# Kernel tuning notes

Hardware: AMD Instinct MI355X
Metric: run time of the kernel (lower is better)

## Reference

```python
import jax, jax.numpy as jnp
import numpy as np
import math

B, T, C, H = 2, 2048, 1024, 16
DH = C // H  # head_dim = 64
NEG = -1000000000.0


def _rope_freqs(T, half, base=10000.0):
    inv = 1.0 / (base ** (np.arange(0, half, dtype=np.float32) * 2.0 / (2 * half)))
    ang = np.arange(T, dtype=np.float32)[:, None] * inv[None, :]  # (T, half)
    return np.cos(ang)[None, :, None, :], np.sin(ang)[None, :, None, :]


def setup_inputs() -> dict:
    key = jax.random.key(0)
    ks = jax.random.split(key, 9)
    s = 1.0 / math.sqrt(C)
    cos, sin = _rope_freqs(T, DH // 2)
    return {
        "x": jax.random.normal(ks[0], (B, T, C), jnp.float32),
        "mask": jnp.tril(jnp.ones((T, T), bool))[None, None],  # (1,1,T,T) causal
        "freqs_cos": jnp.asarray(cos),
        "freqs_sin": jnp.asarray(sin),
        "wq": jax.random.normal(ks[1], (C, C), jnp.float32) * s,
        "bq": jnp.zeros((C,), jnp.float32),
        "wk": jax.random.normal(ks[2], (C, C), jnp.float32) * s,
        "bk": jnp.zeros((C,), jnp.float32),
        "wv": jax.random.normal(ks[3], (C, C), jnp.float32) * s,
        "bv": jnp.zeros((C,), jnp.float32),
        "wo": jax.random.normal(ks[4], (C, C), jnp.float32) * s,
        "bo": jnp.zeros((C,), jnp.float32),
    }


def _apply_rope(x, cos, sin):
    # x: (B, T, H, D); cos/sin: (1, T, 1, D/2)
    xr, xi = x[..., 0::2], x[..., 1::2]
    rr = xr * cos - xi * sin
    ri = xr * sin + xi * cos
    b, t, h, _ = x.shape
    return jnp.stack([rr, ri], axis=-1).reshape(b, t, h, x.shape[-1])


def reference(x, mask, freqs_cos, freqs_sin, wq, bq, wk, bk, wv, bv, wo, bo):
    b, t, c = x.shape
    q = (x @ wq + bq).reshape(b, t, H, DH)
    k = (x @ wk + bk).reshape(b, t, H, DH)
    v = (x @ wv + bv).reshape(b, t, H, DH)
    q = _apply_rope(q, freqs_cos, freqs_sin)
    k = _apply_rope(k, freqs_cos, freqs_sin)
    scores = jnp.einsum('bqhd,bkhd->bhqk', q, k) / math.sqrt(DH)
    scores = jnp.where(mask, scores, NEG)
    probs = jax.nn.softmax(scores, axis=-1)  # dropout is identity (deterministic)
    out = jnp.einsum('bhqk,bkhd->bqhd', probs, v).reshape(b, t, c)
    return out @ wo + bo
```

## Files before the change

### kernel.cpp

```cpp
#include <hip/hip_runtime.h>
#include <hip/hip_bf16.h>


typedef __attribute__((ext_vector_type(8))) short bf16x8;
typedef __attribute__((ext_vector_type(4))) float f32x4;
typedef unsigned short u16;

#define DEV __device__ __forceinline__

#define GLDS16(g, l)                                                        \
  __builtin_amdgcn_global_load_lds(                                         \
      (const __attribute__((address_space(1))) void*)(g),                   \
      (__attribute__((address_space(3))) void*)(l), 16, 0, 0)

DEV u16 f2bf(float f) {
  __hip_bfloat16 h = __float2bfloat16(f);
  u16 u; __builtin_memcpy(&u, &h, 2); return u;
}

__global__ __launch_bounds__(256) void k_cvt(const float* __restrict__ in,
                                             u16* __restrict__ out) {
  int i = (blockIdx.x * 256 + threadIdx.x) * 8;
  float4 a = *(const float4*)(in + i);
  float4 b = *(const float4*)(in + i + 4);
  union { u16 us[8]; uint4 v; } pk;
  pk.us[0] = f2bf(a.x); pk.us[1] = f2bf(a.y); pk.us[2] = f2bf(a.z); pk.us[3] = f2bf(a.w);
  pk.us[4] = f2bf(b.x); pk.us[5] = f2bf(b.y); pk.us[6] = f2bf(b.z); pk.us[7] = f2bf(b.w);
  *(uint4*)(out + i) = pk.v;
}

__global__ __launch_bounds__(256) void k_trw(const float* __restrict__ wq,
                                             const float* __restrict__ wk,
                                             const float* __restrict__ wv,
                                             const float* __restrict__ wo,
                                             u16* __restrict__ Wt,
                                             u16* __restrict__ Wot) {
  __shared__ float tile[32][33];
  const int z = blockIdx.z;
  const float* src = (z == 0) ? wq : (z == 1) ? wk : (z == 2) ? wv : wo;
  u16* dst = (z < 3) ? (Wt + (size_t)z * 1024 * 1024) : Wot;
  const int n0 = blockIdx.x * 32, k0 = blockIdx.y * 32;
  const int tx = threadIdx.x & 31, ty = threadIdx.x >> 5;
#pragma unroll
  for (int rr = 0; rr < 4; ++rr) {
    int k = ty + rr * 8;
    tile[k][tx] = src[(size_t)(k0 + k) * 1024 + n0 + tx];
  }
  __syncthreads();
#pragma unroll
  for (int rr = 0; rr < 4; ++rr) {
    int n = ty + rr * 8;
    dst[(size_t)(n0 + n) * 1024 + k0 + tx] = f2bf(tile[tx][n]);
  }
}

__global__ __launch_bounds__(256) void k_trv(const u16* __restrict__ Vg,
                                             u16* __restrict__ Vt) {
  __shared__ u16 tile[64][72];
  const int tid = threadIdx.x;
  const int bh = blockIdx.y;
  const int t0 = blockIdx.x * 64;
  const int r = tid >> 2, q = tid & 3;
  const u16* src = &Vg[((size_t)bh * 2048 + t0 + r) * 64 + q * 16];
  uint4 u0 = *(const uint4*)src;
  uint4 u1 = *(const uint4*)(src + 8);
  *(uint4*)&tile[r][q * 16] = u0;
  *(uint4*)&tile[r][q * 16 + 8] = u1;
  __syncthreads();
  const int d = tid >> 2;
  union { u16 us[16]; uint4 v[2]; } pk;
#pragma unroll
  for (int i = 0; i < 16; ++i) pk.us[i] = tile[q * 16 + i][d];
  u16* dst = &Vt[((size_t)bh * 64 + d) * 2048 + t0 + q * 16];
  *(uint4*)dst = pk.v[0];
  *(uint4*)(dst + 8) = pk.v[1];
}

template <int EPI>
__global__ __launch_bounds__(256) void k_gemm(
    const u16* __restrict__ A, const u16* __restrict__ Bt,
    const float* __restrict__ b0, const float* __restrict__ b1,
    const float* __restrict__ b2, const float* __restrict__ fcos,
    const float* __restrict__ fsin, u16* __restrict__ Qg, u16* __restrict__ Kg,
    u16* __restrict__ Vg, float* __restrict__ outF) {
  __shared__ u16 As[128 * 32];
  __shared__ u16 Bs[128 * 32];
  const int tid = threadIdx.x, lane = tid & 63, wid = tid >> 6;
  const int wm = wid >> 1, wn = wid & 1;
  const int lr = lane & 15, lg = lane >> 4;
  const int m0 = blockIdx.y * 128, n0 = blockIdx.x * 128;
  const int K = 1024;
  f32x4 acc[4][4] = {};

  const int srcChunk = (lane & 3) ^ ((lane >> 3) & 3);
  const int rowIn = lane >> 2;
  const int seg0 = wid * 2;
  const u16* aSrc0 = &A[(size_t)(m0 + seg0 * 16 + rowIn) * K + srcChunk * 8];
  const u16* aSrc1 = aSrc0 + 16 * K;
  const u16* bSrc0 = &Bt[(size_t)(n0 + seg0 * 16 + rowIn) * K + srcChunk * 8];
  const u16* bSrc1 = bSrc0 + 16 * K;
  u16* aDst0 = &As[seg0 * 512];
  u16* aDst1 = &As[seg0 * 512 + 512];
  u16* bDst0 = &Bs[seg0 * 512];
  u16* bDst1 = &Bs[seg0 * 512 + 512];

  const int slot = (lg ^ ((lr >> 1) & 3)) * 8;

  for (int kt = 0; kt < 32; ++kt) {
    const int ko = kt * 32;
    GLDS16(aSrc0 + ko, aDst0);
    GLDS16(aSrc1 + ko, aDst1);
    GLDS16(bSrc0 + ko, bDst0);
    GLDS16(bSrc1 + ko, bDst1);
    __syncthreads();
    bf16x8 af[4], bfr[4];
#pragma unroll
    for (int i = 0; i < 4; ++i)
      af[i] = *(const bf16x8*)&As[(wm * 64 + i * 16 + lr) * 32 + slot];
#pragma unroll
    for (int j = 0; j < 4; ++j)
      bfr[j] = *(const bf16x8*)&Bs[(wn * 64 + j * 16 + lr) * 32 + slot];
#pragma unroll
    for (int i = 0; i < 4; ++i)
#pragma unroll
      for (int j = 0; j < 4; ++j)
        acc[i][j] = __builtin_amdgcn_mfma_f32_16x16x32_bf16(af[i], bfr[j],
                                                            acc[i][j], 0, 0, 0);
    __syncthreads();
  }

  if constexpr (EPI == 0) {
#pragma unroll
    for (int i = 0; i < 4; ++i) {
#pragma unroll
      for (int j = 0; j < 4; ++j) {
        f32x4 v = acc[i][j];
        int n = n0 + wn * 64 + j * 16 + lr;
        int mat = n >> 10, nn = n & 1023;
        int h = nn >> 6, d = nn & 63;
        float bval = (mat == 0 ? b0 : (mat == 1 ? b1 : b2))[nn];
        int mb = m0 + wm * 64 + i * 16 + lg * 4;
        if (mat < 2) {
          int p = d >> 1;
          float sgn = (d & 1) ? 1.0f : -1.0f;
          u16* dst = (mat == 0) ? Qg : Kg;
#pragma unroll
          for (int r = 0; r < 4; ++r) {
            int m = mb + r, t = m & 2047, b = m >> 11;
            float val = v[r] + bval;
            float c = fcos[t * 32 + p], s = fsin[t * 32 + p];
            float partner = __shfl_xor(val, 1);
            float rv = val * c + sgn * partner * s;
            dst[((size_t)(b * 16 + h) * 2048 + t) * 64 + d] = f2bf(rv);
          }
        } else {
#pragma unroll
          for (int r = 0; r < 4; ++r) {
            int m = mb + r, t = m & 2047, b = m >> 11;
            Vg[((size_t)(b * 16 + h) * 2048 + t) * 64 + d] = f2bf(v[r] + bval);
          }
        }
      }
    }
  } else {
#pragma unroll
    for (int i = 0; i < 4; ++i) {
#pragma unroll
      for (int j = 0; j < 4; ++j) {
        int n = n0 + wn * 64 + j * 16 + lr;
        float bval = b0[n];
        int mb = m0 + wm * 64 + i * 16 + lg * 4;
#pragma unroll
        for (int r = 0; r < 4; ++r)
          outF[(size_t)(mb + r) * 1024 + n] = acc[i][j][r] + bval;
      }
    }
  }
}

__global__ __launch_bounds__(256, 2) void k_attn(const u16* __restrict__ Qg,
                                                 const u16* __restrict__ Kg,
                                                 const u16* __restrict__ Vt,
                                                 u16* __restrict__ Ab) {
  __shared__ u16 PA_lds[4][16][72];
  __shared__ u16 PB_lds[4][16][72];
  const int tid = threadIdx.x, lane = tid & 63, w = tid >> 6;
  const int lr = lane & 15, lg = lane >> 4;
  const int iA = blockIdx.x;
  const int iB = 31 - iA;
  const int bh = blockIdx.y;
  const size_t qkbase = (size_t)bh * 2048 * 64;
  const int qrowA = iA * 64 + w * 16;
  const int qrowB = iB * 64 + w * 16;

  bf16x8 aQA[2], aQB[2];
#pragma unroll
  for (int c = 0; c < 2; ++c) {
    aQA[c] = *(const bf16x8*)&Qg[qkbase + (size_t)(qrowA + lr) * 64 + lg * 8 + c * 32];
    aQB[c] = *(const bf16x8*)&Qg[qkbase + (size_t)(qrowB + lr) * 64 + lg * 8 + c * 32];
  }

  f32x4 accA[4] = {}, accB[4] = {};
  float mA[4], lA[4], mB[4], lB[4];
#pragma unroll
  for (int r = 0; r < 4; ++r) { mA[r] = -1e30f; lA[r] = 0.f; mB[r] = -1e30f; lB[r] = 0.f; }

  bf16x8 k0buf[4][2], k1buf[4][2];
#pragma unroll
  for (int nt = 0; nt < 4; ++nt) {
    const u16* kp = &Kg[qkbase + (size_t)(nt * 16 + lr) * 64 + lg * 8];
    k0buf[nt][0] = *(const bf16x8*)kp;
    k0buf[nt][1] = *(const bf16x8*)(kp + 32);
  }

  auto chain = [&](float (&p)[4][4], float (&m_run)[4], float (&l_run)[4],
                   f32x4 (&acc_o)[4], u16 (&P_lds)[4][16][72]) {
    float pm[4], alpha[4], rs[4];
#pragma unroll
    for (int r = 0; r < 4; ++r)
      pm[r] = fmaxf(fmaxf(p[0][r], p[1][r]), fmaxf(p[2][r], p[3][r]));
#pragma unroll
    for (int off = 1; off < 16; off <<= 1)
#pragma unroll
      for (int r = 0; r < 4; ++r) pm[r] = fmaxf(pm[r], __shfl_xor(pm[r], off));
#pragma unroll
    for (int r = 0; r < 4; ++r) {
      float mn = fmaxf(m_run[r], pm[r]);
      alpha[r] = __expf(m_run[r] - mn);
      m_run[r] = mn;
    }
#pragma unroll
    for (int nt = 0; nt < 4; ++nt)
#pragma unroll
      for (int r = 0; r < 4; ++r) p[nt][r] = __expf(p[nt][r] - m_run[r]);
#pragma unroll
    for (int r = 0; r < 4; ++r) rs[r] = (p[0][r] + p[1][r]) + (p[2][r] + p[3][r]);
#pragma unroll
    for (int off = 1; off < 16; off <<= 1)
#pragma unroll
      for (int r = 0; r < 4; ++r) rs[r] += __shfl_xor(rs[r], off);
#pragma unroll
    for (int r = 0; r < 4; ++r) l_run[r] = l_run[r] * alpha[r] + rs[r];
#pragma unroll
    for (int j = 0; j < 4; ++j)
#pragma unroll
      for (int r = 0; r < 4; ++r) acc_o[j][r] *= alpha[r];
#pragma unroll
    for (int nt = 0; nt < 4; ++nt)
#pragma unroll
      for (int r = 0; r < 4; ++r)
        P_lds[w][lg * 4 + r][nt * 16 + lr] = f2bf(p[nt][r]);
  };

  auto step = [&](bf16x8 (&kcur)[4][2], bf16x8 (&knxt)[4][2], int kt) {
    const int kv0 = kt * 64;
    const bool doA = (kt <= iA);
    f32x4 sB[4], sA[4];
#pragma unroll
    for (int nt = 0; nt < 4; ++nt) {
      f32x4 s = {};
      s = __builtin_amdgcn_mfma_f32_16x16x32_bf16(aQB[0], kcur[nt][0], s, 0, 0, 0);
      s = __builtin_amdgcn_mfma_f32_16x16x32_bf16(aQB[1], kcur[nt][1], s, 0, 0, 0);
      sB[nt] = s;
    }
    if (doA) {
#pragma unroll
      for (int nt = 0; nt < 4; ++nt) {
        f32x4 s = {};
        s = __builtin_amdgcn_mfma_f32_16x16x32_bf16(aQA[0], kcur[nt][0], s, 0, 0, 0);
        s = __builtin_amdgcn_mfma_f32_16x16x32_bf16(aQA[1], kcur[nt][1], s, 0, 0, 0);
        sA[nt] = s;
      }
    }
    if (kt < iB) {
#pragma unroll
      for (int nt = 0; nt < 4; ++nt) {
        const u16* kp = &Kg[qkbase + (size_t)(kv0 + 64 + nt * 16 + lr) * 64 + lg * 8];
        knxt[nt][0] = *(const bf16x8*)kp;
        knxt[nt][1] = *(const bf16x8*)(kp + 32);
      }
    }
    bf16x8 vc[4][2];
#pragma unroll
    for (int j = 0; j < 4; ++j) {
      const u16* vp = &Vt[(size_t)(bh * 64 + j * 16 + lr) * 2048 + kv0 + lg * 8];
      vc[j][0] = *(const bf16x8*)vp;
      vc[j][1] = *(const bf16x8*)(vp + 32);
    }
    float pB[4][4], pA[4][4];
#pragma unroll
    for (int nt = 0; nt < 4; ++nt)
#pragma unroll
      for (int r = 0; r < 4; ++r) {
        float xB = sB[nt][r] * 0.125f;
        if (kt == iB && (kv0 + nt * 16 + lr > qrowB + lg * 4 + r)) xB = -1e30f;
        pB[nt][r] = xB;
      }
    if (doA) {
#pragma unroll
      for (int nt = 0; nt < 4; ++nt)
#pragma unroll
        for (int r = 0; r < 4; ++r) {
          float xA = sA[nt][r] * 0.125f;
          if (kt == iA && (kv0 + nt * 16 + lr > qrowA + lg * 4 + r)) xA = -1e30f;
          pA[nt][r] = xA;
        }
    }
    chain(pB, mB, lB, accB, PB_lds);
    if (doA) chain(pA, mA, lA, accA, PA_lds);
    asm volatile("s_waitcnt lgkmcnt(0)" ::: "memory");
    __builtin_amdgcn_sched_barrier(0);
    bf16x8 aPB0 = *(const bf16x8*)&PB_lds[w][lr][lg * 8];
    bf16x8 aPB1 = *(const bf16x8*)&PB_lds[w][lr][lg * 8 + 32];
#pragma unroll
    for (int j = 0; j < 4; ++j) {
      accB[j] = __builtin_amdgcn_mfma_f32_16x16x32_bf16(aPB0, vc[j][0], accB[j], 0, 0, 0);
      accB[j] = __builtin_amdgcn_mfma_f32_16x16x32_bf16(aPB1, vc[j][1], accB[j], 0, 0, 0);
    }
    if (doA) {
      bf16x8 aPA0 = *(const bf16x8*)&PA_lds[w][lr][lg * 8];
      bf16x8 aPA1 = *(const bf16x8*)&PA_lds[w][lr][lg * 8 + 32];
#pragma unroll
      for (int j = 0; j < 4; ++j) {
        accA[j] = __builtin_amdgcn_mfma_f32_16x16x32_bf16(aPA0, vc[j][0], accA[j], 0, 0, 0);
        accA[j] = __builtin_amdgcn_mfma_f32_16x16x32_bf16(aPA1, vc[j][1], accA[j], 0, 0, 0);
      }
    }
  };

  int kt = 0;
  while (true) {
    step(k0buf, k1buf, kt);
    ++kt; if (kt > iB) break;
    step(k1buf, k0buf, kt);
    ++kt; if (kt > iB) break;
  }

  const int b = bh >> 4, h = bh & 15;
#pragma unroll
  for (int j = 0; j < 4; ++j)
#pragma unroll
    for (int r = 0; r < 4; ++r) {
      int qA = qrowA + lg * 4 + r;
      int qB = qrowB + lg * 4 + r;
      Ab[(size_t)(b * 2048 + qA) * 1024 + h * 64 + j * 16 + lr] = f2bf(accA[j][r] / lA[r]);
      Ab[(size_t)(b * 2048 + qB) * 1024 + h * 64 + j * 16 + lr] = f2bf(accB[j][r] / lB[r]);
    }
}

extern "C" void kernel_launch(void* const* d_in, const int* in_sizes, int n_in,
                              void* d_out, int out_size, void* d_ws,
                              size_t ws_size, hipStream_t stream) {
  (void)in_sizes; (void)n_in; (void)out_size; (void)ws_size;
  const float* x = (const float*)d_in[0];
  const float* fcos = (const float*)d_in[2];
  const float* fsin = (const float*)d_in[3];
  const float* wq = (const float*)d_in[4];
  const float* bq = (const float*)d_in[5];
  const float* wk = (const float*)d_in[6];
  const float* bk = (const float*)d_in[7];
  const float* wv = (const float*)d_in[8];
  const float* bv = (const float*)d_in[9];
  const float* wo = (const float*)d_in[10];
  const float* bo = (const float*)d_in[11];
  float* out = (float*)d_out;
  char* ws = (char*)d_ws;
  const size_t MB = 1024 * 1024;
  u16* Xb  = (u16*)(ws);
  u16* Wt  = (u16*)(ws + 8 * MB);
  u16* Wot = (u16*)(ws + 14 * MB);
  u16* Qg  = (u16*)(ws + 16 * MB);
  u16* Kg  = (u16*)(ws + 24 * MB);
  u16* Vg  = (u16*)(ws + 32 * MB);
  u16* Vt  = (u16*)(ws + 40 * MB);
  u16* Ab  = Xb;

  k_cvt<<<2048, 256, 0, stream>>>(x, Xb);
  k_trw<<<dim3(32, 32, 4), 256, 0, stream>>>(wq, wk, wv, wo, Wt, Wot);
  k_gemm<0><<<dim3(24, 32), 256, 0, stream>>>(Xb, Wt, bq, bk, bv, fcos, fsin,
                                              Qg, Kg, Vg, nullptr);
  k_trv<<<dim3(32, 32), 256, 0, stream>>>(Vg, Vt);
  k_attn<<<dim3(16, 32), 256, 0, stream>>>(Qg, Kg, Vt, Ab);
  k_gemm<1><<<dim3(8, 32), 256, 0, stream>>>(Ab, Wot, bo, nullptr, nullptr,
                                             nullptr, nullptr, nullptr, nullptr,
                                             nullptr, out);
}
```

Measured before the change: 288.2 us.

## Split KV tiles across two warp halves in attention and merge partial softmax

The attention block grows from 256 to 512 threads. The two halves of the warps take even and odd KV tiles, and each prefetches K two tiles ahead. After the loop, the odd half writes its partial accumulators and running max/sum to LDS, reusing the P buffers. The even half then rescales and merges them before writing the output. This doubles the waves working on each query pair, which should raise latency hiding and shorten per-block serial work; the costs are an extra LDS combine step and two barriers. The tighter launch bound of (512,4) may also cap registers hard enough to cause spills.

```diff
diff --git a/kernel.cpp b/kernel.cpp
--- a/kernel.cpp
+++ b/kernel.cpp
@@ -178,20 +178,26 @@
   }
 }
 
-__global__ __launch_bounds__(256, 2) void k_attn(const u16* __restrict__ Qg,
+struct CombW {
+  float acc[2][16][65];
+  float ml[2][2][16];
+};
+__global__ __launch_bounds__(512, 4) void k_attn(const u16* __restrict__ Qg,
                                                  const u16* __restrict__ Kg,
                                                  const u16* __restrict__ Vt,
                                                  u16* __restrict__ Ab) {
-  __shared__ u16 PA_lds[4][16][72];
-  __shared__ u16 PB_lds[4][16][72];
+  __shared__ u16 P_all[2][8][16][72];
   const int tid = threadIdx.x, lane = tid & 63, w = tid >> 6;
+  const int wl = w & 3, half = w >> 2;
   const int lr = lane & 15, lg = lane >> 4;
   const int iA = blockIdx.x;
   const int iB = 31 - iA;
   const int bh = blockIdx.y;
   const size_t qkbase = (size_t)bh * 2048 * 64;
-  const int qrowA = iA * 64 + w * 16;
-  const int qrowB = iB * 64 + w * 16;
+  const int qrowA = iA * 64 + wl * 16;
+  const int qrowB = iB * 64 + wl * 16;
+  u16 (*PA)[72] = P_all[0][w];
+  u16 (*PB)[72] = P_all[1][w];
 
   bf16x8 aQA[2], aQB[2];
 #pragma unroll
@@ -208,13 +214,13 @@
   bf16x8 k0buf[4][2], k1buf[4][2];
 #pragma unroll
   for (int nt = 0; nt < 4; ++nt) {
-    const u16* kp = &Kg[qkbase + (size_t)(nt * 16 + lr) * 64 + lg * 8];
+    const u16* kp = &Kg[qkbase + (size_t)(half * 64 + nt * 16 + lr) * 64 + lg * 8];
     k0buf[nt][0] = *(const bf16x8*)kp;
     k0buf[nt][1] = *(const bf16x8*)(kp + 32);
   }
 
   auto chain = [&](float (&p)[4][4], float (&m_run)[4], float (&l_run)[4],
-                   f32x4 (&acc_o)[4], u16 (&P_lds)[4][16][72]) {
+                   f32x4 (&acc_o)[4], u16 (*P)[72]) {
     float pm[4], alpha[4], rs[4];
 #pragma unroll
     for (int r = 0; r < 4; ++r)
@@ -249,7 +255,7 @@
     for (int nt = 0; nt < 4; ++nt)
 #pragma unroll
       for (int r = 0; r < 4; ++r)
-        P_lds[w][lg * 4 + r][nt * 16 + lr] = f2bf(p[nt][r]);
+        P[lg * 4 + r][nt * 16 + lr] = f2bf(p[nt][r]);
   };
 
   auto step = [&](bf16x8 (&kcur)[4][2], bf16x8 (&knxt)[4][2], int kt) {
@@ -272,10 +278,10 @@
         sA[nt] = s;
       }
     }
-    if (kt < iB) {
+    if (kt + 2 <= iB) {
 #pragma unroll
       for (int nt = 0; nt < 4; ++nt) {
-        const u16* kp = &Kg[qkbase + (size_t)(kv0 + 64 + nt * 16 + lr) * 64 + lg * 8];
+        const u16* kp = &Kg[qkbase + (size_t)(kv0 + 128 + nt * 16 + lr) * 64 + lg * 8];
         knxt[nt][0] = *(const bf16x8*)kp;
         knxt[nt][1] = *(const bf16x8*)(kp + 32);
       }
@@ -306,20 +312,20 @@
           pA[nt][r] = xA;
         }
     }
-    chain(pB, mB, lB, accB, PB_lds);
-    if (doA) chain(pA, mA, lA, accA, PA_lds);
+    chain(pB, mB, lB, accB, PB);
+    if (doA) chain(pA, mA, lA, accA, PA);
     asm volatile("s_waitcnt lgkmcnt(0)" ::: "memory");
     __builtin_amdgcn_sched_barrier(0);
-    bf16x8 aPB0 = *(const bf16x8*)&PB_lds[w][lr][lg * 8];
-    bf16x8 aPB1 = *(const bf16x8*)&PB_lds[w][lr][lg * 8 + 32];
+    bf16x8 aPB0 = *(const bf16x8*)&PB[lr][lg * 8];
+    bf16x8 aPB1 = *(const bf16x8*)&PB[lr][lg * 8 + 32];
 #pragma unroll
     for (int j = 0; j < 4; ++j) {
       accB[j] = __builtin_amdgcn_mfma_f32_16x16x32_bf16(aPB0, vc[j][0], accB[j], 0, 0, 0);
       accB[j] = __builtin_amdgcn_mfma_f32_16x16x32_bf16(aPB1, vc[j][1], accB[j], 0, 0, 0);
     }
     if (doA) {
-      bf16x8 aPA0 = *(const bf16x8*)&PA_lds[w][lr][lg * 8];
-      bf16x8 aPA1 = *(const bf16x8*)&PA_lds[w][lr][lg * 8 + 32];
+      bf16x8 aPA0 = *(const bf16x8*)&PA[lr][lg * 8];
+      bf16x8 aPA1 = *(const bf16x8*)&PA[lr][lg * 8 + 32];
 #pragma unroll
       for (int j = 0; j < 4; ++j) {
         accA[j] = __builtin_amdgcn_mfma_f32_16x16x32_bf16(aPA0, vc[j][0], accA[j], 0, 0, 0);
@@ -328,24 +334,59 @@
     }
   };
 
-  int kt = 0;
-  while (true) {
+  int kt = half;
+  while (kt <= iB) {
     step(k0buf, k1buf, kt);
-    ++kt; if (kt > iB) break;
+    kt += 2; if (kt > iB) break;
     step(k1buf, k0buf, kt);
-    ++kt; if (kt > iB) break;
-  }
-
-  const int b = bh >> 4, h = bh & 15;
-#pragma unroll
-  for (int j = 0; j < 4; ++j)
+    kt += 2;
+  }
+
+  __syncthreads();
+  CombW* comb = (CombW*)&P_all[0][0][0][0];
+  if (half == 1) {
+    CombW& cw = comb[wl];
 #pragma unroll
     for (int r = 0; r < 4; ++r) {
-      int qA = qrowA + lg * 4 + r;
-      int qB = qrowB + lg * 4 + r;
-      Ab[(size_t)(b * 2048 + qA) * 1024 + h * 64 + j * 16 + lr] = f2bf(accA[j][r] / lA[r]);
-      Ab[(size_t)(b * 2048 + qB) * 1024 + h * 64 + j * 16 + lr] = f2bf(accB[j][r] / lB[r]);
-    }
+      int row = lg * 4 + r;
+      cw.ml[0][0][row] = mA[r]; cw.ml[0][1][row] = lA[r];
+      cw.ml[1][0][row] = mB[r]; cw.ml[1][1][row] = lB[r];
+#pragma unroll
+      for (int j = 0; j < 4; ++j) {
+        cw.acc[0][row][j * 16 + lr] = accA[j][r];
+        cw.acc[1][row][j * 16 + lr] = accB[j][r];
+      }
+    }
+  }
+  __syncthreads();
+  if (half == 0) {
+    CombW& cw = comb[wl];
+    const int b = bh >> 4, h = bh & 15;
+#pragma unroll
+    for (int r = 0; r < 4; ++r) {
+      int row = lg * 4 + r;
+      float m1 = cw.ml[0][0][row], l1 = cw.ml[0][1][row];
+      float mm = fmaxf(mA[r], m1);
+      float w0 = __expf(mA[r] - mm), w1 = __expf(m1 - mm);
+      float lT = lA[r] * w0 + l1 * w1;
+      int qA = qrowA + row;
+#pragma unroll
+      for (int j = 0; j < 4; ++j) {
+        float o = accA[j][r] * w0 + cw.acc[0][row][j * 16 + lr] * w1;
+        Ab[(size_t)(b * 2048 + qA) * 1024 + h * 64 + j * 16 + lr] = f2bf(o / lT);
+      }
+      m1 = cw.ml[1][0][row]; l1 = cw.ml[1][1][row];
+      mm = fmaxf(mB[r], m1);
+      w0 = __expf(mB[r] - mm); w1 = __expf(m1 - mm);
+      lT = lB[r] * w0 + l1 * w1;
+      int qB = qrowB + row;
+#pragma unroll
+      for (int j = 0; j < 4; ++j) {
+        float o = accB[j][r] * w0 + cw.acc[1][row][j * 16 + lr] * w1;
+        Ab[(size_t)(b * 2048 + qB) * 1024 + h * 64 + j * 16 + lr] = f2bf(o / lT);
+      }
+    }
+  }
 }
 
 extern "C" void kernel_launch(void* const* d_in, const int* in_sizes, int n_in,
@@ -380,7 +421,7 @@
   k_gemm<0><<<dim3(24, 32), 256, 0, stream>>>(Xb, Wt, bq, bk, bv, fcos, fsin,
                                               Qg, Kg, Vg, nullptr);
   k_trv<<<dim3(32, 32), 256, 0, stream>>>(Vg, Vt);
-  k_attn<<<dim3(16, 32), 256, 0, stream>>>(Qg, Kg, Vt, Ab);
+  k_attn<<<dim3(16, 32), 512, 0, stream>>>(Qg, Kg, Vt, Ab);
   k_gemm<1><<<dim3(8, 32), 256, 0, stream>>>(Ab, Wot, bo, nullptr, nullptr,
                                              nullptr, nullptr, nullptr, nullptr,
                                              nullptr, out);
```

Result: slower. 565.5 us (+96.2%).
